# Kernel optimization log

Hardware: AMD Instinct MI355X
Metric: run time of the kernel (lower is better)

## Reference

```python
import jax, jax.numpy as jnp
import numpy as np

B, C, P, T, H = 4, 256, 1024, 64, 8
D = C // H
SCALE = float(np.sqrt(D * T))


def setup_inputs() -> dict:
    key = jax.random.key(0)
    ks = jax.random.split(key, 7)
    s = 1.0 / np.sqrt(C)
    return {
        "x": jax.random.normal(ks[0], (B, C, P, T), dtype=jnp.float32),
        "Wk": jax.random.uniform(ks[1], (C, C), dtype=jnp.float32, minval=-s, maxval=s),
        "bk": jax.random.uniform(ks[2], (C,), dtype=jnp.float32, minval=-s, maxval=s),
        "Wq": jax.random.uniform(ks[3], (C, C), dtype=jnp.float32, minval=-s, maxval=s),
        "bq": jax.random.uniform(ks[4], (C,), dtype=jnp.float32, minval=-s, maxval=s),
        "Wv": jax.random.uniform(ks[5], (C, C), dtype=jnp.float32, minval=-s, maxval=s),
        "bv": jax.random.uniform(ks[6], (C,), dtype=jnp.float32, minval=-s, maxval=s),
    }


def _proj_split(x, W, b):
    # 1x1 conv == channel-mixing linear; then split heads: b (h d) p t -> b h d p t
    y = jnp.einsum('bcpt,oc->bopt', x, W) + b[None, :, None, None]
    Bs, _, Ps, Ts = y.shape
    return y.reshape(Bs, H, D, Ps, Ts)


def reference(x, Wk, bk, Wq, bq, Wv, bv):
    k = _proj_split(x, Wk, bk)
    q = _proj_split(x, Wq, bq)
    v = _proj_split(x, Wv, bv)
    # contract jointly over d and t
    energy = jnp.einsum('bhdpt,bhdqt->bhpq', k, q)
    attn = jax.nn.softmax(energy / SCALE, axis=-1)
    out = jnp.einsum('bhpq,bhdpt->bhdqt', attn, v)
    # merge heads: b h d q t -> b (h d) q t
    return out.reshape(B, C, P, T)
```

## Files before the change

kernel.cpp:

```cpp
#include <hip/hip_runtime.h>
#include <cstdint>
#include <cstddef>

#define NB 4
#define NC 256
#define NP 1024
#define NT 64
#define NH 8
#define ND 32
#define NF 2048
#define NPT 65536
#define KQV_ELEMS 67108864ull
#define INV_SCALE 0.022097086912079608f
#define MHAT 4.0f

typedef unsigned short u16;
typedef __bf16 bf16x8 __attribute__((ext_vector_type(8)));
typedef short  s16x8  __attribute__((ext_vector_type(8)));
typedef short  s16x4  __attribute__((ext_vector_type(4)));
typedef float  f32x4  __attribute__((ext_vector_type(4)));

__device__ __forceinline__ u16 f2bf(float f) {
  unsigned u = __builtin_bit_cast(unsigned, f);
  u += 0x7fffu + ((u >> 16) & 1u);
  return (u16)(u >> 16);
}
__device__ __forceinline__ float bf2f(u16 h) {
  unsigned u = ((unsigned)h) << 16;
  return __builtin_bit_cast(float, u);
}
__device__ __forceinline__ int swz(int row) { return ((row ^ (row >> 3)) & 7) << 4; }

#define GLOAD_LDS16(gp, lp) __builtin_amdgcn_global_load_lds( \
    (const __attribute__((address_space(1))) void*)(gp),      \
    (__attribute__((address_space(3))) void*)(lp), 16, 0, 0)

__device__ __forceinline__ f32x4 mfma16(bf16x8 a, bf16x8 b, f32x4 c) {
  return __builtin_amdgcn_mfma_f32_16x16x32_bf16(a, b, c, 0, 0, 0);
}

__global__ __launch_bounds__(256) void wcast_kernel(
    const float* __restrict__ Wk, const float* __restrict__ Wq,
    const float* __restrict__ Wv, u16* __restrict__ wbf)
{
  int pj = blockIdx.y;
  const float* W = (pj == 0) ? Wk : ((pj == 1) ? Wq : Wv);
  int idx = blockIdx.x * 1024 + threadIdx.x * 4;
  float4 v = *(const float4*)(W + idx);
  s16x4 pk;
  pk[0] = (short)f2bf(v.x); pk[1] = (short)f2bf(v.y);
  pk[2] = (short)f2bf(v.z); pk[3] = (short)f2bf(v.w);
  *(s16x4*)(wbf + (size_t)pj * 65536 + idx) = pk;
}

__global__ __launch_bounds__(256, 2) void xcast_kernel(
    const float* __restrict__ x, u16* __restrict__ xT)
{
  int ptt = blockIdx.x;
  int ct  = blockIdx.y;
  int b   = blockIdx.z;
  __shared__ __align__(16) u16 L[64 * 64];
  int tid = threadIdx.x;
#pragma unroll
  for (int i = 0; i < 4; i++) {
    int cl  = i * 16 + (tid >> 4);
    int ptl = (tid & 15) * 4;
    float4 v = *(const float4*)(x + ((size_t)(b * NC + ct * 64 + cl)) * NPT +
                                ptt * 64 + ptl);
    s16x4 pk;
    pk[0] = (short)f2bf(v.x); pk[1] = (short)f2bf(v.y);
    pk[2] = (short)f2bf(v.z); pk[3] = (short)f2bf(v.w);
    *(s16x4*)((char*)L + ((cl * 128 + ptl * 2) ^ swz(cl))) = pk;
  }
  __syncthreads();
#pragma unroll
  for (int i = 0; i < 2; i++) {
    int ptl = i * 32 + (tid >> 3);
    int c8  = (tid & 7) * 8;
    s16x8 v;
#pragma unroll
    for (int j = 0; j < 8; j++) {
      int row = c8 + j;
      v[j] = (short)*(const u16*)((char*)L + ((row * 128 + ptl * 2) ^ swz(row)));
    }
    *(s16x8*)(xT + ((size_t)b * NPT + (size_t)ptt * 64 + ptl) * NC + ct * 64 + c8) = v;
  }
}

__global__ __launch_bounds__(256, 2) void transpose_kernel(
    const u16* __restrict__ in, u16* __restrict__ outp,
    const float* __restrict__ pstats)
{
  int ft = blockIdx.x;
  int pt = blockIdx.y;
  int slab = blockIdx.z;
  __shared__ __align__(16) u16 L[64 * 64];
  int t = threadIdx.x;
  const u16* ip = in + (size_t)slab * NP * NF;
#pragma unroll
  for (int i = 0; i < 2; i++) {
    int pl = i * 32 + (t >> 3);
    int c8 = (t & 7) * 8;
    s16x8 v = *(const s16x8*)(ip + (size_t)(pt * 64 + pl) * NF + ft * 64 + c8);
    *(s16x8*)((char*)L + ((pl * 128 + c8 * 2) ^ swz(pl))) = v;
  }
  __syncthreads();
  int p8 = (t & 7) * 8;
  const float* pp = pstats + slab * 4096 + pt * 64 + p8;
  float sc[8];
#pragma unroll
  for (int j2 = 0; j2 < 8; j2++)
    sc[j2] = 1.0f / (pp[j2] + pp[j2 + 1024] + pp[j2 + 2048] + pp[j2 + 3072]);
  u16* op = outp + (size_t)slab * NP * NF;
#pragma unroll
  for (int i = 0; i < 2; i++) {
    int fl = i * 32 + (t >> 3);
    s16x8 v;
#pragma unroll
    for (int j2 = 0; j2 < 8; j2++) {
      int row = p8 + j2;
      u16 raw = *(const u16*)((char*)L + ((row * 128 + fl * 2) ^ swz(row)));
      v[j2] = (short)f2bf(bf2f(raw) * sc[j2]);
    }
    *(s16x8*)(op + (size_t)(ft * 64 + fl) * NP + pt * 64 + p8) = v;
  }
}

#define PJSTG(TT) do {                                                         \
    GLOAD_LDS16(Ag + (size_t)psrow * NC + (TT) * 32 + psg * 8,                 \
                L + ((((TT) & 1) * 32768 + pdst) >> 1));                       \
    GLOAD_LDS16(Bg + (size_t)psrow * NC + (TT) * 32 + psg * 8,                 \
                L + ((((TT) & 1) * 32768 + 16384 + pdst) >> 1));               \
  } while (0)

#define PJBODY(J, WAITASM, DOSTG) do {                                         \
    if (DOSTG) PJSTG((J) + 1);                                                 \
    __builtin_amdgcn_sched_barrier(0);                                         \
    asm volatile(WAITASM ::: "memory");                                        \
    __builtin_amdgcn_s_barrier();                                              \
    __builtin_amdgcn_sched_barrier(0);                                         \
    {                                                                          \
      const int bb = ((J) & 1) * 32768;                                        \
      bf16x8 af[4], bfr[4];                                                    \
      _Pragma("unroll")                                                        \
      for (int mf = 0; mf < 4; mf++)                                           \
        af[mf] = *(const bf16x8*)((char*)L + bb + baseA + mf * 1024);          \
      _Pragma("unroll")                                                        \
      for (int nf = 0; nf < 4; nf++)                                           \
        bfr[nf] = *(const bf16x8*)((char*)L + bb + 16384 + baseB + nf * 1024); \
      __builtin_amdgcn_s_setprio(1);                                           \
      _Pragma("unroll")                                                        \
      for (int mf = 0; mf < 4; mf++)                                           \
        _Pragma("unroll")                                                      \
        for (int nf = 0; nf < 4; nf++)                                         \
          acc[mf][nf] = mfma16(af[mf], bfr[nf], acc[mf][nf]);                  \
      __builtin_amdgcn_s_setprio(0);                                           \
    }                                                                          \
    __builtin_amdgcn_sched_barrier(0);                                         \
    asm volatile("s_waitcnt lgkmcnt(0)" ::: "memory");                         \
    __builtin_amdgcn_s_barrier();                                              \
    asm volatile("" ::: "memory");                                             \
    __builtin_amdgcn_sched_barrier(0);                                         \
  } while (0)

__global__ __launch_bounds__(1024) void proj1024_kernel(
    const u16* __restrict__ wbf, const u16* __restrict__ xT,
    const float* __restrict__ bk, const float* __restrict__ bq,
    const float* __restrict__ bv, u16* __restrict__ kqv)
{
  __shared__ __align__(16) u16 L[32768];
  int d0 = blockIdx.x;
  int b  = blockIdx.y;
  int xcd = d0 & 7, r = d0 >> 3;
  int pj  = r % 3, tch = r / 3;
  int ptile = tch * 8 + xcd;
  const float* bias = (pj == 0) ? bk : ((pj == 1) ? bq : bv);
  u16* outb = kqv + (size_t)pj * KQV_ELEMS;
  const int n0 = ptile * 256;

  const u16* Ag = wbf + (size_t)pj * 65536;
  const u16* Bg = xT + ((size_t)b * NPT + (size_t)n0) * NC;

  const int tid  = threadIdx.x;
  const int lane = tid & 63;
  const int wv   = tid >> 6;
  const int wr = wv >> 2, wc = wv & 3;

  const int psrow = tid >> 2;
  const int psg   = (lane & 3) ^ ((lane >> 3) & 3);
  const int pdst  = wv * 1024;

  const int ra0 = wr * 64 + (lane & 15);
  const int rb0 = wc * 64 + (lane & 15);
  const int gk  = lane >> 4;
  const int baseA = ra0 * 64 + ((gk ^ ((ra0 >> 1) & 3)) << 4);
  const int baseB = rb0 * 64 + ((gk ^ ((rb0 >> 1) & 3)) << 4);

  f32x4 acc[4][4];
#pragma unroll
  for (int a = 0; a < 4; a++)
#pragma unroll
    for (int c = 0; c < 4; c++) acc[a][c] = (f32x4){0.f, 0.f, 0.f, 0.f};

  PJSTG(0);
  __builtin_amdgcn_sched_barrier(0);

  PJBODY(0, "s_waitcnt vmcnt(2)", 1);
  PJBODY(1, "s_waitcnt vmcnt(2)", 1);
  PJBODY(2, "s_waitcnt vmcnt(2)", 1);
  PJBODY(3, "s_waitcnt vmcnt(2)", 1);
  PJBODY(4, "s_waitcnt vmcnt(2)", 1);
  PJBODY(5, "s_waitcnt vmcnt(2)", 1);
  PJBODY(6, "s_waitcnt vmcnt(2)", 1);
  PJBODY(7, "s_waitcnt vmcnt(0)", 0);

#pragma unroll
  for (int mf = 0; mf < 4; mf++) {
#pragma unroll
    for (int jj = 0; jj < 4; jj++) {
      int o = wr * 64 + mf * 16 + (lane >> 4) * 4 + jj;
      float bsv = bias[o];
      int hh = o >> 5, dd = o & 31;
#pragma unroll
      for (int nf = 0; nf < 4; nf++) {
        int n = n0 + wc * 64 + nf * 16 + (lane & 15);
        int p = n >> 6, t = n & 63;
        outb[((size_t)(b * NH + hh) * NP + p) * NF + dd * 64 + t] =
            f2bf(acc[mf][nf][jj] + bsv);
      }
    }
  }
}

#define STG2(BASE, TT) do {                                                    \
    GLOAD_LDS16(Ag + (size_t)grow[0] * KT + (TT) * 32 + gcol[0],               \
                L + (((BASE) + W0) >> 1));                                     \
    GLOAD_LDS16(Ag + (size_t)grow[1] * KT + (TT) * 32 + gcol[1],               \
                L + (((BASE) + W1) >> 1));                                     \
    GLOAD_LDS16(Bg + (size_t)grow[2] * KT + (TT) * 32 + gcol[2],               \
                L + (((BASE) + 16384 + W0) >> 1));                             \
    GLOAD_LDS16(Bg + (size_t)grow[3] * KT + (TT) * 32 + gcol[3],               \
                L + (((BASE) + 16384 + W1) >> 1));                             \
  } while (0)

#define KBODY2(CB, WAITASM, DOSTG, SB, TT) do {                                \
    if (DOSTG) STG2((SB) * 32768, TT);                                         \
    __builtin_amdgcn_sched_barrier(0);                                         \
    asm volatile(WAITASM ::: "memory");                                        \
    __builtin_amdgcn_s_barrier();                                              \
    __builtin_amdgcn_sched_barrier(0);                                         \
    {                                                                          \
      const int bb = (CB) * 32768;                                             \
      bf16x8 a_[8], b_[4];                                                     \
      _Pragma("unroll")                                                        \
      for (int mf = 0; mf < 8; mf++)                                           \
        a_[mf] = *(const bf16x8*)((const char*)L + bb + baseA + mf * 1024);    \
      _Pragma("unroll")                                                        \
      for (int nf = 0; nf < 4; nf++)                                           \
        b_[nf] = *(const bf16x8*)((const char*)L + bb + 16384 + baseB +        \
                                  nf * 1024);                                  \
      asm volatile("s_waitcnt lgkmcnt(0)" ::: "memory");                       \
      __builtin_amdgcn_sched_barrier(0);                                       \
      __builtin_amdgcn_s_setprio(1);                                           \
      _Pragma("unroll")                                                        \
      for (int mf = 0; mf < 8; mf++)                                           \
        _Pragma("unroll")                                                      \
        for (int nf = 0; nf < 4; nf++)                                         \
          acc[mf][nf] = mfma16(a_[mf], b_[nf], acc[mf][nf]);                   \
      __builtin_amdgcn_s_setprio(0);                                           \
    }                                                                          \
    __builtin_amdgcn_sched_barrier(0);                                         \
    __builtin_amdgcn_s_barrier();                                              \
    asm volatile("" ::: "memory");                                             \
    __builtin_amdgcn_sched_barrier(0);                                         \
  } while (0)

template <int KT>
__device__ __forceinline__ void core256(const u16* __restrict__ Ag,
                                        const u16* __restrict__ Bg,
                                        u16* L, f32x4 acc[8][4])
{
  constexpr int NKT = KT / 32;
  const int tid  = threadIdx.x;
  const int lane = tid & 63;
  const int wv   = tid >> 6;
  const int wr = wv >> 2, wc = wv & 3;

  int grow[4], gcol[4];
#pragma unroll
  for (int i = 0; i < 4; i++) {
    int oi   = (tid + (i & 1) * 512) * 16;
    int loff = oi ^ (((oi >> 7) & 3) << 4);
    grow[i] = loff >> 6;
    gcol[i] = (loff & 63) >> 1;
  }
  const int W0 = wv * 1024;
  const int W1 = wv * 1024 + 8192;

  const int rowA  = wr * 128 + (lane & 15);
  const int baseA = rowA * 64 + ((((lane >> 4)) ^ ((rowA >> 1) & 3)) << 4);
  const int rowB  = wc * 64 + (lane & 15);
  const int baseB = rowB * 64 + ((((lane >> 4)) ^ ((rowB >> 1) & 3)) << 4);

  STG2(0, 0);
  STG2(32768, 1);
  __builtin_amdgcn_sched_barrier(0);

  int cb = 0, sb = 2;
  for (int j = 0; j < NKT - 2; ++j) {
    KBODY2(cb, "s_waitcnt vmcnt(8)", 1, sb, j + 2);
    cb = (cb == 2) ? 0 : cb + 1;
    sb = (sb == 2) ? 0 : sb + 1;
  }
  KBODY2(cb, "s_waitcnt vmcnt(4)", 0, 0, 0);
  cb = (cb == 2) ? 0 : cb + 1;
  KBODY2(cb, "s_waitcnt vmcnt(0)", 0, 0, 0);
}

__global__ __launch_bounds__(512, 2) void qk256_kernel(
    const u16* __restrict__ kb, const u16* __restrict__ qb,
    u16* __restrict__ Pb, float* __restrict__ pstats)
{
  extern __shared__ u16 L[];
  int bid = blockIdx.x;
  int xcd = bid & 7, r = bid >> 3;
  int bh  = xcd * 4 + (r >> 4);
  int til = r & 15;
  int mt  = til >> 2, nt = til & 3;

  const u16* Ag = qb + (size_t)bh * NP * NF + (size_t)mt * 256 * NF;
  const u16* Bg = kb + (size_t)bh * NP * NF + (size_t)nt * 256 * NF;

  f32x4 acc[8][4];
#pragma unroll
  for (int a = 0; a < 8; a++)
#pragma unroll
    for (int c = 0; c < 4; c++) acc[a][c] = (f32x4){0.f, 0.f, 0.f, 0.f};

  core256<NF>(Ag, Bg, L, acc);

  const int tid  = threadIdx.x;
  const int lane = tid & 63, wv = tid >> 6;
  const int wr = wv >> 2, wc = wv & 3;
  u16* Pp = Pb + (size_t)bh * NP * NP;

  float l4[4] = {0.f, 0.f, 0.f, 0.f};
#pragma unroll
  for (int mf = 0; mf < 8; mf++)
#pragma unroll
    for (int jj = 0; jj < 4; jj++) {
      int m = mt * 256 + wr * 128 + mf * 16 + (lane >> 4) * 4 + jj;
#pragma unroll
      for (int nf = 0; nf < 4; nf++) {
        int n = nt * 256 + wc * 64 + nf * 16 + (lane & 15);
        float e = __expf(acc[mf][nf][jj] * INV_SCALE - MHAT);
        l4[nf] += e;
        Pp[(size_t)m * NP + n] = f2bf(e);
      }
    }

#pragma unroll
  for (int nf = 0; nf < 4; nf++) {
    l4[nf] += __shfl_xor(l4[nf], 16);
    l4[nf] += __shfl_xor(l4[nf], 32);
  }
  float* st = (float*)L;
  __syncthreads();
  if (lane < 16) {
#pragma unroll
    for (int nf = 0; nf < 4; nf++)
      st[wr * 256 + wc * 64 + nf * 16 + lane] = l4[nf];
  }
  __syncthreads();
  if (tid < 256) {
    float s = st[tid] + st[256 + tid];
    pstats[((bh * 4 + mt) << 10) + nt * 256 + tid] = s;
  }
}

__global__ __launch_bounds__(512, 2) void av256_kernel(
    const u16* __restrict__ Pb, const u16* __restrict__ Vt, float* __restrict__ out)
{
  extern __shared__ u16 L[];
  int bid = blockIdx.x;
  int xcd = bid & 7, r = bid >> 3;
  int bh  = xcd * 4 + (r >> 5);
  int til = r & 31;
  int mt  = til >> 3, ntf = til & 7;

  const u16* Ag = Pb + (size_t)bh * NP * NP + (size_t)mt * 256 * NP;
  const u16* Bg = Vt + (size_t)bh * NF * NP + (size_t)ntf * 256 * NP;

  f32x4 acc[8][4];
#pragma unroll
  for (int a = 0; a < 8; a++)
#pragma unroll
    for (int c = 0; c < 4; c++) acc[a][c] = (f32x4){0.f, 0.f, 0.f, 0.f};

  core256<NP>(Ag, Bg, L, acc);

  const int lane = threadIdx.x & 63, wv = threadIdx.x >> 6;
  const int wr = wv >> 2, wc = wv & 3;
  int b = bh >> 3, h = bh & 7;
#pragma unroll
  for (int mf = 0; mf < 8; mf++)
#pragma unroll
    for (int jj = 0; jj < 4; jj++) {
      int m = mt * 256 + wr * 128 + mf * 16 + (lane >> 4) * 4 + jj;
#pragma unroll
      for (int nf = 0; nf < 4; nf++) {
        int n = ntf * 256 + wc * 64 + nf * 16 + (lane & 15);
        int dd = n >> 6, t = n & 63;
        out[((size_t)(b * NC + h * ND + dd) * NP + m) * NT + t] = acc[mf][nf][jj];
      }
    }
}

extern "C" void kernel_launch(void* const* d_in, const int* in_sizes, int n_in,
                              void* d_out, int out_size, void* d_ws, size_t ws_size,
                              hipStream_t stream)
{
  if (ws_size < 4ull * KQV_ELEMS * sizeof(u16)) return;

  const float* x  = (const float*)d_in[0];
  const float* Wk = (const float*)d_in[1];
  const float* bk = (const float*)d_in[2];
  const float* Wq = (const float*)d_in[3];
  const float* bq = (const float*)d_in[4];
  const float* Wv = (const float*)d_in[5];
  const float* bv = (const float*)d_in[6];

  u16* kb = (u16*)d_ws;
  u16* qb = kb + KQV_ELEMS;
  u16* vb = kb + 2 * KQV_ELEMS;
  u16* Pb = kb + 3 * KQV_ELEMS;
  float* pstats = (float*)(Pb + 33554432);
  u16* vt = kb;

  u16* xT  = (u16*)d_out;
  u16* wbf = xT + KQV_ELEMS;

  (void)hipFuncSetAttribute((const void*)qk256_kernel,
                            hipFuncAttributeMaxDynamicSharedMemorySize, 98304);
  (void)hipFuncSetAttribute((const void*)av256_kernel,
                            hipFuncAttributeMaxDynamicSharedMemorySize, 98304);

  wcast_kernel<<<dim3(64, 3), 256, 0, stream>>>(Wk, Wq, Wv, wbf);
  xcast_kernel<<<dim3(1024, 4, 4), 256, 0, stream>>>(x, xT);
  proj1024_kernel<<<dim3(768, 4), 1024, 0, stream>>>(wbf, xT, bk, bq, bv, kb);
  qk256_kernel<<<dim3(512), 512, 98304, stream>>>(kb, qb, Pb, pstats);
  transpose_kernel<<<dim3(32, 16, 32), 256, 0, stream>>>(vb, vt, pstats);
  av256_kernel<<<dim3(1024), 512, 98304, stream>>>(Pb, vt, (float*)d_out);
}
```

Measured before the change: 661.2 us.

## Switch QK and AV GEMMs to 1024-thread blocks with shared double-buffered core

Replaces the 512-thread, 3-stage-pipelined 256x256 GEMM core used by the QK and AV kernels with the 1024-thread, 2-stage double-buffered core already used by the projection. Each wave now computes a 64x64 subtile instead of 128x64, using 32KB static LDS instead of 96KB dynamic. This halves per-wave accumulator registers and doubles waves per tile to raise occupancy and latency hiding. The trade-off is a shallower prefetch pipeline, more per-wave LDS fragment reads relative to MFMA work, and one block per CU instead of two.

```diff
diff --git a/kernel.cpp b/kernel.cpp
--- a/kernel.cpp
+++ b/kernel.cpp
@@ -126,21 +126,21 @@
   }
 }
 
-#define PJSTG(TT) do {                                                         \
-    GLOAD_LDS16(Ag + (size_t)psrow * NC + (TT) * 32 + psg * 8,                 \
+#define G1STG(KT, TT) do {                                                     \
+    GLOAD_LDS16(Ag + (size_t)psrow * (KT) + (size_t)(TT) * 32 + psg * 8,       \
                 L + ((((TT) & 1) * 32768 + pdst) >> 1));                       \
-    GLOAD_LDS16(Bg + (size_t)psrow * NC + (TT) * 32 + psg * 8,                 \
+    GLOAD_LDS16(Bg + (size_t)psrow * (KT) + (size_t)(TT) * 32 + psg * 8,       \
                 L + ((((TT) & 1) * 32768 + 16384 + pdst) >> 1));               \
   } while (0)
 
-#define PJBODY(J, WAITASM, DOSTG) do {                                         \
-    if (DOSTG) PJSTG((J) + 1);                                                 \
+#define G1BODY(KT, PAR, J, WAITASM, DOSTG) do {                                \
+    if (DOSTG) G1STG(KT, (J) + 1);                                             \
     __builtin_amdgcn_sched_barrier(0);                                         \
     asm volatile(WAITASM ::: "memory");                                        \
     __builtin_amdgcn_s_barrier();                                              \
     __builtin_amdgcn_sched_barrier(0);                                         \
     {                                                                          \
-      const int bb = ((J) & 1) * 32768;                                        \
+      const int bb = (PAR) * 32768;                                            \
       bf16x8 af[4], bfr[4];                                                    \
       _Pragma("unroll")                                                        \
       for (int mf = 0; mf < 4; mf++)                                           \
@@ -163,6 +163,25 @@
     __builtin_amdgcn_sched_barrier(0);                                         \
   } while (0)
 
+template <int KT>
+__device__ __forceinline__ void core1024(const u16* __restrict__ Ag,
+                                         const u16* __restrict__ Bg,
+                                         u16* L, f32x4 acc[4][4],
+                                         int psrow, int psg, int pdst,
+                                         int baseA, int baseB)
+{
+  constexpr int NKT = KT / 32;
+  G1STG(KT, 0);
+  __builtin_amdgcn_sched_barrier(0);
+#pragma unroll 1
+  for (int j = 0; j < NKT - 2; j += 2) {
+    G1BODY(KT, 0, j,     "s_waitcnt vmcnt(2)", 1);
+    G1BODY(KT, 1, j + 1, "s_waitcnt vmcnt(2)", 1);
+  }
+  G1BODY(KT, 0, NKT - 2, "s_waitcnt vmcnt(2)", 1);
+  G1BODY(KT, 1, NKT - 1, "s_waitcnt vmcnt(0)", 0);
+}
+
 __global__ __launch_bounds__(1024) void proj1024_kernel(
     const u16* __restrict__ wbf, const u16* __restrict__ xT,
     const float* __restrict__ bk, const float* __restrict__ bq,
@@ -202,17 +221,7 @@
 #pragma unroll
     for (int c = 0; c < 4; c++) acc[a][c] = (f32x4){0.f, 0.f, 0.f, 0.f};
 
-  PJSTG(0);
-  __builtin_amdgcn_sched_barrier(0);
-
-  PJBODY(0, "s_waitcnt vmcnt(2)", 1);
-  PJBODY(1, "s_waitcnt vmcnt(2)", 1);
-  PJBODY(2, "s_waitcnt vmcnt(2)", 1);
-  PJBODY(3, "s_waitcnt vmcnt(2)", 1);
-  PJBODY(4, "s_waitcnt vmcnt(2)", 1);
-  PJBODY(5, "s_waitcnt vmcnt(2)", 1);
-  PJBODY(6, "s_waitcnt vmcnt(2)", 1);
-  PJBODY(7, "s_waitcnt vmcnt(0)", 0);
+  core1024<NC>(Ag, Bg, L, acc, psrow, psg, pdst, baseA, baseB);
 
 #pragma unroll
   for (int mf = 0; mf < 4; mf++) {
@@ -232,96 +241,11 @@
   }
 }
 
-#define STG2(BASE, TT) do {                                                    \
-    GLOAD_LDS16(Ag + (size_t)grow[0] * KT + (TT) * 32 + gcol[0],               \
-                L + (((BASE) + W0) >> 1));                                     \
-    GLOAD_LDS16(Ag + (size_t)grow[1] * KT + (TT) * 32 + gcol[1],               \
-                L + (((BASE) + W1) >> 1));                                     \
-    GLOAD_LDS16(Bg + (size_t)grow[2] * KT + (TT) * 32 + gcol[2],               \
-                L + (((BASE) + 16384 + W0) >> 1));                             \
-    GLOAD_LDS16(Bg + (size_t)grow[3] * KT + (TT) * 32 + gcol[3],               \
-                L + (((BASE) + 16384 + W1) >> 1));                             \
-  } while (0)
-
-#define KBODY2(CB, WAITASM, DOSTG, SB, TT) do {                                \
-    if (DOSTG) STG2((SB) * 32768, TT);                                         \
-    __builtin_amdgcn_sched_barrier(0);                                         \
-    asm volatile(WAITASM ::: "memory");                                        \
-    __builtin_amdgcn_s_barrier();                                              \
-    __builtin_amdgcn_sched_barrier(0);                                         \
-    {                                                                          \
-      const int bb = (CB) * 32768;                                             \
-      bf16x8 a_[8], b_[4];                                                     \
-      _Pragma("unroll")                                                        \
-      for (int mf = 0; mf < 8; mf++)                                           \
-        a_[mf] = *(const bf16x8*)((const char*)L + bb + baseA + mf * 1024);    \
-      _Pragma("unroll")                                                        \
-      for (int nf = 0; nf < 4; nf++)                                           \
-        b_[nf] = *(const bf16x8*)((const char*)L + bb + 16384 + baseB +        \
-                                  nf * 1024);                                  \
-      asm volatile("s_waitcnt lgkmcnt(0)" ::: "memory");                       \
-      __builtin_amdgcn_sched_barrier(0);                                       \
-      __builtin_amdgcn_s_setprio(1);                                           \
-      _Pragma("unroll")                                                        \
-      for (int mf = 0; mf < 8; mf++)                                           \
-        _Pragma("unroll")                                                      \
-        for (int nf = 0; nf < 4; nf++)                                         \
-          acc[mf][nf] = mfma16(a_[mf], b_[nf], acc[mf][nf]);                   \
-      __builtin_amdgcn_s_setprio(0);                                           \
-    }                                                                          \
-    __builtin_amdgcn_sched_barrier(0);                                         \
-    __builtin_amdgcn_s_barrier();                                              \
-    asm volatile("" ::: "memory");                                             \
-    __builtin_amdgcn_sched_barrier(0);                                         \
-  } while (0)
-
-template <int KT>
-__device__ __forceinline__ void core256(const u16* __restrict__ Ag,
-                                        const u16* __restrict__ Bg,
-                                        u16* L, f32x4 acc[8][4])
-{
-  constexpr int NKT = KT / 32;
-  const int tid  = threadIdx.x;
-  const int lane = tid & 63;
-  const int wv   = tid >> 6;
-  const int wr = wv >> 2, wc = wv & 3;
-
-  int grow[4], gcol[4];
-#pragma unroll
-  for (int i = 0; i < 4; i++) {
-    int oi   = (tid + (i & 1) * 512) * 16;
-    int loff = oi ^ (((oi >> 7) & 3) << 4);
-    grow[i] = loff >> 6;
-    gcol[i] = (loff & 63) >> 1;
-  }
-  const int W0 = wv * 1024;
-  const int W1 = wv * 1024 + 8192;
-
-  const int rowA  = wr * 128 + (lane & 15);
-  const int baseA = rowA * 64 + ((((lane >> 4)) ^ ((rowA >> 1) & 3)) << 4);
-  const int rowB  = wc * 64 + (lane & 15);
-  const int baseB = rowB * 64 + ((((lane >> 4)) ^ ((rowB >> 1) & 3)) << 4);
-
-  STG2(0, 0);
-  STG2(32768, 1);
-  __builtin_amdgcn_sched_barrier(0);
-
-  int cb = 0, sb = 2;
-  for (int j = 0; j < NKT - 2; ++j) {
-    KBODY2(cb, "s_waitcnt vmcnt(8)", 1, sb, j + 2);
-    cb = (cb == 2) ? 0 : cb + 1;
-    sb = (sb == 2) ? 0 : sb + 1;
-  }
-  KBODY2(cb, "s_waitcnt vmcnt(4)", 0, 0, 0);
-  cb = (cb == 2) ? 0 : cb + 1;
-  KBODY2(cb, "s_waitcnt vmcnt(0)", 0, 0, 0);
-}
-
-__global__ __launch_bounds__(512, 2) void qk256_kernel(
+__global__ __launch_bounds__(1024) void qk1024_kernel(
     const u16* __restrict__ kb, const u16* __restrict__ qb,
     u16* __restrict__ Pb, float* __restrict__ pstats)
 {
-  extern __shared__ u16 L[];
+  __shared__ __align__(16) u16 L[32768];
   int bid = blockIdx.x;
   int xcd = bid & 7, r = bid >> 3;
   int bh  = xcd * 4 + (r >> 4);
@@ -331,25 +255,36 @@
   const u16* Ag = qb + (size_t)bh * NP * NF + (size_t)mt * 256 * NF;
   const u16* Bg = kb + (size_t)bh * NP * NF + (size_t)nt * 256 * NF;
 
-  f32x4 acc[8][4];
-#pragma unroll
-  for (int a = 0; a < 8; a++)
+  const int tid  = threadIdx.x;
+  const int lane = tid & 63;
+  const int wv   = tid >> 6;
+  const int wr = wv >> 2, wc = wv & 3;
+
+  const int psrow = tid >> 2;
+  const int psg   = (lane & 3) ^ ((lane >> 3) & 3);
+  const int pdst  = wv * 1024;
+
+  const int ra0 = wr * 64 + (lane & 15);
+  const int rb0 = wc * 64 + (lane & 15);
+  const int gk  = lane >> 4;
+  const int baseA = ra0 * 64 + ((gk ^ ((ra0 >> 1) & 3)) << 4);
+  const int baseB = rb0 * 64 + ((gk ^ ((rb0 >> 1) & 3)) << 4);
+
+  f32x4 acc[4][4];
+#pragma unroll
+  for (int a = 0; a < 4; a++)
 #pragma unroll
     for (int c = 0; c < 4; c++) acc[a][c] = (f32x4){0.f, 0.f, 0.f, 0.f};
 
-  core256<NF>(Ag, Bg, L, acc);
-
-  const int tid  = threadIdx.x;
-  const int lane = tid & 63, wv = tid >> 6;
-  const int wr = wv >> 2, wc = wv & 3;
+  core1024<NF>(Ag, Bg, L, acc, psrow, psg, pdst, baseA, baseB);
+
   u16* Pp = Pb + (size_t)bh * NP * NP;
-
   float l4[4] = {0.f, 0.f, 0.f, 0.f};
 #pragma unroll
-  for (int mf = 0; mf < 8; mf++)
+  for (int mf = 0; mf < 4; mf++)
 #pragma unroll
     for (int jj = 0; jj < 4; jj++) {
-      int m = mt * 256 + wr * 128 + mf * 16 + (lane >> 4) * 4 + jj;
+      int m = mt * 256 + wr * 64 + mf * 16 + (lane >> 4) * 4 + jj;
 #pragma unroll
       for (int nf = 0; nf < 4; nf++) {
         int n = nt * 256 + wc * 64 + nf * 16 + (lane & 15);
@@ -373,15 +308,15 @@
   }
   __syncthreads();
   if (tid < 256) {
-    float s = st[tid] + st[256 + tid];
+    float s = st[tid] + st[256 + tid] + st[512 + tid] + st[768 + tid];
     pstats[((bh * 4 + mt) << 10) + nt * 256 + tid] = s;
   }
 }
 
-__global__ __launch_bounds__(512, 2) void av256_kernel(
+__global__ __launch_bounds__(1024) void av1024_kernel(
     const u16* __restrict__ Pb, const u16* __restrict__ Vt, float* __restrict__ out)
 {
-  extern __shared__ u16 L[];
+  __shared__ __align__(16) u16 L[32768];
   int bid = blockIdx.x;
   int xcd = bid & 7, r = bid >> 3;
   int bh  = xcd * 4 + (r >> 5);
@@ -391,22 +326,35 @@
   const u16* Ag = Pb + (size_t)bh * NP * NP + (size_t)mt * 256 * NP;
   const u16* Bg = Vt + (size_t)bh * NF * NP + (size_t)ntf * 256 * NP;
 
-  f32x4 acc[8][4];
-#pragma unroll
-  for (int a = 0; a < 8; a++)
+  const int tid  = threadIdx.x;
+  const int lane = tid & 63;
+  const int wv   = tid >> 6;
+  const int wr = wv >> 2, wc = wv & 3;
+
+  const int psrow = tid >> 2;
+  const int psg   = (lane & 3) ^ ((lane >> 3) & 3);
+  const int pdst  = wv * 1024;
+
+  const int ra0 = wr * 64 + (lane & 15);
+  const int rb0 = wc * 64 + (lane & 15);
+  const int gk  = lane >> 4;
+  const int baseA = ra0 * 64 + ((gk ^ ((ra0 >> 1) & 3)) << 4);
+  const int baseB = rb0 * 64 + ((gk ^ ((rb0 >> 1) & 3)) << 4);
+
+  f32x4 acc[4][4];
+#pragma unroll
+  for (int a = 0; a < 4; a++)
 #pragma unroll
     for (int c = 0; c < 4; c++) acc[a][c] = (f32x4){0.f, 0.f, 0.f, 0.f};
 
-  core256<NP>(Ag, Bg, L, acc);
-
-  const int lane = threadIdx.x & 63, wv = threadIdx.x >> 6;
-  const int wr = wv >> 2, wc = wv & 3;
+  core1024<NP>(Ag, Bg, L, acc, psrow, psg, pdst, baseA, baseB);
+
   int b = bh >> 3, h = bh & 7;
 #pragma unroll
-  for (int mf = 0; mf < 8; mf++)
+  for (int mf = 0; mf < 4; mf++)
 #pragma unroll
     for (int jj = 0; jj < 4; jj++) {
-      int m = mt * 256 + wr * 128 + mf * 16 + (lane >> 4) * 4 + jj;
+      int m = mt * 256 + wr * 64 + mf * 16 + (lane >> 4) * 4 + jj;
 #pragma unroll
       for (int nf = 0; nf < 4; nf++) {
         int n = ntf * 256 + wc * 64 + nf * 16 + (lane & 15);
@@ -440,15 +388,10 @@
   u16* xT  = (u16*)d_out;
   u16* wbf = xT + KQV_ELEMS;
 
-  (void)hipFuncSetAttribute((const void*)qk256_kernel,
-                            hipFuncAttributeMaxDynamicSharedMemorySize, 98304);
-  (void)hipFuncSetAttribute((const void*)av256_kernel,
-                            hipFuncAttributeMaxDynamicSharedMemorySize, 98304);
-
   wcast_kernel<<<dim3(64, 3), 256, 0, stream>>>(Wk, Wq, Wv, wbf);
   xcast_kernel<<<dim3(1024, 4, 4), 256, 0, stream>>>(x, xT);
   proj1024_kernel<<<dim3(768, 4), 1024, 0, stream>>>(wbf, xT, bk, bq, bv, kb);
-  qk256_kernel<<<dim3(512), 512, 98304, stream>>>(kb, qb, Pb, pstats);
+  qk1024_kernel<<<dim3(512), 1024, 0, stream>>>(kb, qb, Pb, pstats);
   transpose_kernel<<<dim3(32, 16, 32), 256, 0, stream>>>(vb, vt, pstats);
-  av256_kernel<<<dim3(1024), 512, 98304, stream>>>(Pb, vt, (float*)d_out);
-}
+  av1024_kernel<<<dim3(1024), 1024, 0, stream>>>(Pb, vt, (float*)d_out);
+}
```

Result: slower. 681.9 us (+3.1%).
